# Performance work log

Hardware: AMD Instinct MI355X
Metric: run time of the kernel (lower is better)

The kernel has to match this reference:

```python
import jax, jax.numpy as jnp
import numpy as np


def setup_inputs() -> dict:
    key = jax.random.key(0)
    k1, k2, k3, k4 = jax.random.split(key, 4)
    n1, n2, d, num_types = 8192, 8192, 512, 64
    return {
        "input1": jax.random.normal(k1, (n1, d), dtype=jnp.float32),
        "input2": jax.random.normal(k2, (n2, d), dtype=jnp.float32),
        "weight": jax.random.normal(k3, (num_types, d), dtype=jnp.float32),
        "bias": jax.random.uniform(k4, (1,), dtype=jnp.float32),
        "type_index": 3,
    }


def reference(input1, input2, weight, bias, type_index):
    # DistMult score: (input1 * w_r) @ input2^T + bias.
    # Original builds diag(w_r) and does a dense d x d GEMM; the faithful
    # math is an elementwise row-scale followed by one GEMM.
    w_r = weight[type_index]                      # [d]
    scaled = input1 * w_r[None, :]                # [n1, d]
    out = scaled @ input2.T + bias                # [n1, n2]
    return out  # act is identity
```

## Files before the change

### kernel.cpp

```cpp
#include <hip/hip_runtime.h>


#define N1 8192
#define N2 8192
#define DK 512
#define BM 128
#define BN 128
#define BK 32

typedef short bf16x8 __attribute__((ext_vector_type(8)));
typedef float f32x4 __attribute__((ext_vector_type(4)));

__device__ __forceinline__ unsigned short f2bf(float f) {
    unsigned int u = __float_as_uint(f);
    u = (u + 0x7FFFu + ((u >> 16) & 1u)) >> 16;
    return (unsigned short)u;
}

__global__ __launch_bounds__(256) void convert_kernel(
        const float* __restrict__ in1, const float* __restrict__ in2,
        const float* __restrict__ weight, const int* __restrict__ type_index,
        unsigned short* __restrict__ a_bf, unsigned short* __restrict__ b_bf) {
    const int QA = N1 * DK / 4;
    int i = blockIdx.x * blockDim.x + threadIdx.x;
    if (i < QA) {
        float4 v = reinterpret_cast<const float4*>(in1)[i];
        int c4 = i & (DK / 4 - 1);
        float4 w = reinterpret_cast<const float4*>(weight + (size_t)(*type_index) * DK)[c4];
        ushort4 o;
        o.x = f2bf(v.x * w.x);
        o.y = f2bf(v.y * w.y);
        o.z = f2bf(v.z * w.z);
        o.w = f2bf(v.w * w.w);
        reinterpret_cast<ushort4*>(a_bf)[i] = o;
    } else {
        int j = i - QA;
        float4 v = reinterpret_cast<const float4*>(in2)[j];
        ushort4 o;
        o.x = f2bf(v.x);
        o.y = f2bf(v.y);
        o.z = f2bf(v.z);
        o.w = f2bf(v.w);
        reinterpret_cast<ushort4*>(b_bf)[j] = o;
    }
}

__global__ __launch_bounds__(256) void gemm_bt(
        const unsigned short* __restrict__ A, const unsigned short* __restrict__ B,
        const float* __restrict__ bias, float* __restrict__ C) {
    __shared__ __align__(16) unsigned short ldsA[BM * BK];
    __shared__ __align__(16) unsigned short ldsB[BN * BK];

    const int tid  = threadIdx.x;
    const int wave = tid >> 6;
    const int lane = tid & 63;
    const int quad = lane >> 4;
    const int r16  = lane & 15;
    const int wm   = wave & 1;
    const int wn   = wave >> 1;

    const int bm = blockIdx.y * BM;
    const int bn = blockIdx.x * BN;

    f32x4 acc[4][4];
#pragma unroll
    for (int i = 0; i < 4; ++i)
#pragma unroll
        for (int j = 0; j < 4; ++j)
            acc[i][j] = (f32x4){0.f, 0.f, 0.f, 0.f};

    const int srow = wave * 32 + (lane >> 2);
    const int scol = (lane & 3) * 8;
    const unsigned short* ag0 = A + (size_t)(bm + srow) * DK + scol;
    const unsigned short* ag1 = ag0 + 16 * DK;
    const unsigned short* bg0 = B + (size_t)(bn + srow) * DK + scol;
    const unsigned short* bg1 = bg0 + 16 * DK;

    unsigned short* la0 = &ldsA[wave * 1024];
    unsigned short* la1 = &ldsA[wave * 1024 + 512];
    unsigned short* lb0 = &ldsB[wave * 1024];
    unsigned short* lb1 = &ldsB[wave * 1024 + 512];

    for (int kt = 0; kt < DK; kt += BK) {
        __builtin_amdgcn_global_load_lds(ag0 + kt, la0, 16, 0, 0);
        __builtin_amdgcn_global_load_lds(ag1 + kt, la1, 16, 0, 0);
        __builtin_amdgcn_global_load_lds(bg0 + kt, lb0, 16, 0, 0);
        __builtin_amdgcn_global_load_lds(bg1 + kt, lb1, 16, 0, 0);
        __syncthreads();

        bf16x8 af[4], bfr[4];
#pragma unroll
        for (int mi = 0; mi < 4; ++mi)
            af[mi] = *(const bf16x8*)&ldsA[(wm * 64 + mi * 16 + r16) * BK + quad * 8];
#pragma unroll
        for (int ni = 0; ni < 4; ++ni)
            bfr[ni] = *(const bf16x8*)&ldsB[(wn * 64 + ni * 16 + r16) * BK + quad * 8];

#pragma unroll
        for (int mi = 0; mi < 4; ++mi)
#pragma unroll
            for (int ni = 0; ni < 4; ++ni)
                acc[mi][ni] = __builtin_amdgcn_mfma_f32_16x16x32_bf16(
                    af[mi], bfr[ni], acc[mi][ni], 0, 0, 0);
        __syncthreads();
    }

    const float bv = bias[0];
#pragma unroll
    for (int mi = 0; mi < 4; ++mi) {
        const int row0 = bm + wm * 64 + mi * 16 + quad * 4;
#pragma unroll
        for (int ni = 0; ni < 4; ++ni) {
            const int col = bn + wn * 64 + ni * 16 + r16;
#pragma unroll
            for (int r = 0; r < 4; ++r)
                C[(size_t)(row0 + r) * N2 + col] = acc[mi][ni][r] + bv;
        }
    }
}

__global__ void naive_kernel(const float* __restrict__ in1, const float* __restrict__ in2,
                             const float* __restrict__ weight, const int* __restrict__ type_index,
                             const float* __restrict__ bias, float* __restrict__ out) {
    int col = blockIdx.x * 16 + threadIdx.x;
    int row = blockIdx.y * 16 + threadIdx.y;
    const float* wr = weight + (size_t)(*type_index) * DK;
    float s = 0.f;
    for (int k = 0; k < DK; ++k)
        s += in1[(size_t)row * DK + k] * wr[k] * in2[(size_t)col * DK + k];
    out[(size_t)row * N2 + col] = s + bias[0];
}

extern "C" void kernel_launch(void* const* d_in, const int* in_sizes, int n_in,
                              void* d_out, int out_size, void* d_ws, size_t ws_size,
                              hipStream_t stream) {
    const float* in1  = (const float*)d_in[0];
    const float* in2  = (const float*)d_in[1];
    const float* wgt  = (const float*)d_in[2];
    const float* bias = (const float*)d_in[3];
    const int*   tix  = (const int*)d_in[4];
    float* out = (float*)d_out;

    const size_t need = 2ull * (N1 + N2) * DK;
    if (ws_size >= need) {
        unsigned short* a_bf = (unsigned short*)d_ws;
        unsigned short* b_bf = a_bf + (size_t)N1 * DK;

        const int total4 = (N1 + N2) * DK / 4;
        convert_kernel<<<total4 / 256, 256, 0, stream>>>(in1, in2, wgt, tix, a_bf, b_bf);

        dim3 grid(N2 / BN, N1 / BM);
        gemm_bt<<<grid, 256, 0, stream>>>(a_bf, b_bf, bias, out);
    } else {
        dim3 grid(N2 / 16, N1 / 16);
        dim3 blk(16, 16);
        naive_kernel<<<grid, blk, 0, stream>>>(in1, in2, wgt, tix, bias, out);
    }
}
```

Measured before the change: 348.9 us.

## Replace GEMM with 256x256 double-buffered swizzled-LDS kernel with interleaved loads

Adds a new bf16 MFMA GEMM that uses 256x256 output tiles, 512 threads and 128 KB of dynamic LDS. K-tiles of 64 are double-buffered and their async global-to-LDS loads are interleaved between MFMA quarter-blocks, with explicit waitcnt and setprio control. It also XOR-swizzles the LDS layout to reduce bank conflicts and remaps block IDs for L2 locality. The goal is more data reuse per tile and overlap of memory traffic with compute. In exchange, occupancy is lower, register pressure is high, and a hipFuncSetAttribute call is made on every launch.

After: 388.2 us. +11.2%, slower.

```diff
diff --git a/kernel.cpp b/kernel.cpp
--- a/kernel.cpp
+++ b/kernel.cpp
@@ -4,9 +4,12 @@
 #define N1 8192
 #define N2 8192
 #define DK 512
+
 #define BM 128
 #define BN 128
 #define BK 32
+
+#define NT (DK / 64)
 
 typedef short bf16x8 __attribute__((ext_vector_type(8)));
 typedef float f32x4 __attribute__((ext_vector_type(4)));
@@ -45,6 +48,139 @@
     }
 }
 
+#define FENCE() asm volatile("" ::: "memory")
+#define LGKM(n) asm volatile("s_waitcnt lgkmcnt(" #n ")" ::: "memory")
+#define VMC(n)  asm volatile("s_waitcnt vmcnt(" #n ")" ::: "memory")
+#define SB0()   __builtin_amdgcn_sched_barrier(0)
+#define BARR()  do { FENCE(); __builtin_amdgcn_s_barrier(); FENCE(); } while (0)
+
+#define MMAQ(M0, N0)                                                                  \
+    do {                                                                              \
+        __builtin_amdgcn_s_setprio(1);                                                \
+        _Pragma("unroll") for (int mi_ = 0; mi_ < 4; ++mi_)                           \
+        _Pragma("unroll") for (int ni_ = 0; ni_ < 2; ++ni_)                           \
+        _Pragma("unroll") for (int kk_ = 0; kk_ < 2; ++kk_)                           \
+            acc[(M0) + mi_][(N0) + ni_] = __builtin_amdgcn_mfma_f32_16x16x32_bf16(    \
+                af[(M0) + mi_][kk_], bfr[(N0) + ni_][kk_], acc[(M0) + mi_][(N0) + ni_], 0, 0, 0); \
+        __builtin_amdgcn_s_setprio(0);                                                \
+    } while (0)
+
+#define STAGE(srcp, matbase, h, T) do {                                               \
+    char* _d = sm + (matbase) + (((T) & 1) * 32768) + (h) * 16384 + wave * 1024;      \
+    __builtin_amdgcn_global_load_lds(                                                 \
+        (const unsigned int*)((srcp) + (size_t)(T) * 128), (unsigned int*)_d, 16, 0, 0); \
+    __builtin_amdgcn_global_load_lds(                                                 \
+        (const unsigned int*)((srcp) + (size_t)(T) * 128 + 65536),                    \
+        (unsigned int*)(_d + 8192), 16, 0, 0);                                        \
+} while (0)
+
+__global__ __launch_bounds__(512, 2) void gemm_256(
+        const unsigned short* __restrict__ A, const unsigned short* __restrict__ B,
+        const float* __restrict__ bias, float* __restrict__ C) {
+    extern __shared__ char sm[];
+    const int tid  = threadIdx.x;
+    const int wave = tid >> 6;
+    const int lane = tid & 63;
+    const int quad = lane >> 4;
+    const int r16  = lane & 15;
+    const int wm   = wave >> 2;
+    const int wn   = wave & 3;
+
+    const int bid = blockIdx.x;
+    const int swz = (bid & 7) * 128 + (bid >> 3);
+    const int bm = (swz >> 5) * 256;
+    const int bn = (swz & 31) * 256;
+
+    const int rowh = tid >> 3;
+    const int colb = ((tid & 7) * 16) ^ (((tid >> 5) & 1) << 5);
+    const char* sA0 = (const char*)A + ((size_t)(bm +       rowh) * DK) * 2 + colb;
+    const char* sA1 = (const char*)A + ((size_t)(bm + 128 + rowh) * DK) * 2 + colb;
+    const char* sB0 = (const char*)B + ((size_t)(bn +       rowh) * DK) * 2 + colb;
+    const char* sB1 = (const char*)B + ((size_t)(bn + 128 + rowh) * DK) * 2 + colb;
+
+    f32x4 acc[8][4];
+#pragma unroll
+    for (int i = 0; i < 8; ++i)
+#pragma unroll
+        for (int j = 0; j < 4; ++j)
+            acc[i][j] = (f32x4){0.f, 0.f, 0.f, 0.f};
+
+    const int flip32 = ((r16 >> 2) & 1) << 5;
+    const int xoff   = (r16 * 128 + quad * 16) ^ flip32;
+
+    STAGE(sA0, 0,     0, 0); STAGE(sA1, 0,     1, 0);
+    STAGE(sB0, 65536, 0, 0); STAGE(sB1, 65536, 1, 0);
+    STAGE(sA0, 0,     0, 1); STAGE(sA1, 0,     1, 1);
+    STAGE(sB0, 65536, 0, 1);
+    VMC(6);
+    BARR();
+
+#pragma unroll 1
+    for (int t = 0; t < NT; ++t) {
+        const char* bA = sm + ((t & 1) * 32768) + wm * 16384 + xoff;
+        const char* bB = sm + 65536 + ((t & 1) * 32768) + wn * 8192 + xoff;
+        bf16x8 af[8][2], bfr[4][2];
+
+#pragma unroll
+        for (int mi = 0; mi < 8; ++mi) {
+            af[mi][0] = *(const bf16x8*)(bA + mi * 2048);
+            af[mi][1] = *(const bf16x8*)(bA + mi * 2048 + 64);
+        }
+        FENCE();
+#pragma unroll
+        for (int ni = 0; ni < 2; ++ni) {
+            bfr[ni][0] = *(const bf16x8*)(bB + ni * 2048);
+            bfr[ni][1] = *(const bf16x8*)(bB + ni * 2048 + 64);
+        }
+        FENCE();
+#pragma unroll
+        for (int ni = 2; ni < 4; ++ni) {
+            bfr[ni][0] = *(const bf16x8*)(bB + ni * 2048);
+            bfr[ni][1] = *(const bf16x8*)(bB + ni * 2048 + 64);
+        }
+        FENCE();
+        if (t + 1 < NT) STAGE(sB1, 65536, 1, t + 1);
+        BARR();
+        LGKM(4); SB0();
+        MMAQ(0, 0);
+        BARR();
+
+        if (t + 2 < NT) STAGE(sA0, 0, 0, t + 2);
+        BARR();
+        MMAQ(4, 0);
+        BARR();
+
+        if (t + 2 < NT) STAGE(sA1, 0, 1, t + 2);
+        BARR();
+        LGKM(0); SB0();
+        MMAQ(0, 2);
+        BARR();
+
+        if (t + 2 < NT) STAGE(sB0, 65536, 0, t + 2);
+        BARR();
+        MMAQ(4, 2);
+        if (t < NT - 2) { VMC(6); }
+        else if (t == NT - 2) { VMC(0); }
+        BARR();
+    }
+
+    const float bv = bias[0];
+#pragma unroll
+    for (int mi = 0; mi < 8; ++mi) {
+        const int row0 = bm + wm * 128 + mi * 16 + quad * 4;
+#pragma unroll
+        for (int ni = 0; ni < 4; ++ni) {
+            const int col = bn + wn * 64 + ni * 16 + r16;
+#pragma unroll
+            for (int r = 0; r < 4; ++r)
+                C[(size_t)(row0 + r) * N2 + col] = acc[mi][ni][r] + bv;
+        }
+    }
+}
+
+#undef STAGE
+#undef MMAQ
+
 __global__ __launch_bounds__(256) void gemm_bt(
         const unsigned short* __restrict__ A, const unsigned short* __restrict__ B,
         const float* __restrict__ bias, float* __restrict__ C) {
@@ -149,8 +285,15 @@
         const int total4 = (N1 + N2) * DK / 4;
         convert_kernel<<<total4 / 256, 256, 0, stream>>>(in1, in2, wgt, tix, a_bf, b_bf);
 
-        dim3 grid(N2 / BN, N1 / BM);
-        gemm_bt<<<grid, 256, 0, stream>>>(a_bf, b_bf, bias, out);
+        hipError_t e = hipFuncSetAttribute(
+            reinterpret_cast<const void*>(gemm_256),
+            hipFuncAttributeMaxDynamicSharedMemorySize, 131072);
+        if (e == hipSuccess) {
+            gemm_256<<<dim3(1024), dim3(512), 131072, stream>>>(a_bf, b_bf, bias, out);
+        } else {
+            dim3 grid(N2 / BN, N1 / BM);
+            gemm_bt<<<grid, 256, 0, stream>>>(a_bf, b_bf, bias, out);
+        }
     } else {
         dim3 grid(N2 / 16, N1 / 16);
         dim3 blk(16, 16);
```

## Fuse bf16 conversion into a 256x256 register-prefetched MFMA GEMM

Applied to the files above, without the earlier changes.

Replaces the separate convert kernel and bf16 GEMM with one fused kernel. It loads fp32 inputs, scales A by the weight row, converts to bf16 in registers and writes to XOR-swizzled, double-buffered LDS while MFMAs run on the current buffer. The kernel also uses 256x256 tiles with 8 waves, a grid swizzle for L2 locality, and s_setprio around the MFMA blocks. This drops the workspace round trip and one launch. In exchange, fp32 inputs are re-read and re-converted by every tile that uses them, register pressure rises, and 128KB of dynamic LDS limits occupancy.

After: 807.0 us. 131% more time.

```diff
diff --git a/kernel.cpp b/kernel.cpp
--- a/kernel.cpp
+++ b/kernel.cpp
@@ -4,104 +4,336 @@
 #define N1 8192
 #define N2 8192
 #define DK 512
-#define BM 128
-#define BN 128
-#define BK 32
+#define NT 8
 
 typedef short bf16x8 __attribute__((ext_vector_type(8)));
-typedef float f32x4 __attribute__((ext_vector_type(4)));
-
-__device__ __forceinline__ unsigned short f2bf(float f) {
+typedef float f32x4  __attribute__((ext_vector_type(4)));
+
+__device__ __forceinline__ unsigned int f2bf_u(float f) {
     unsigned int u = __float_as_uint(f);
-    u = (u + 0x7FFFu + ((u >> 16) & 1u)) >> 16;
-    return (unsigned short)u;
-}
-
-__global__ __launch_bounds__(256) void convert_kernel(
+    return (u + 0x7FFFu + ((u >> 16) & 1u)) >> 16;
+}
+__device__ __forceinline__ unsigned int pk2(float lo, float hi) {
+    return f2bf_u(lo) | (f2bf_u(hi) << 16);
+}
+
+__global__ __launch_bounds__(512, 2) void fused_gemm_256(
         const float* __restrict__ in1, const float* __restrict__ in2,
         const float* __restrict__ weight, const int* __restrict__ type_index,
-        unsigned short* __restrict__ a_bf, unsigned short* __restrict__ b_bf) {
-    const int QA = N1 * DK / 4;
-    int i = blockIdx.x * blockDim.x + threadIdx.x;
-    if (i < QA) {
-        float4 v = reinterpret_cast<const float4*>(in1)[i];
-        int c4 = i & (DK / 4 - 1);
-        float4 w = reinterpret_cast<const float4*>(weight + (size_t)(*type_index) * DK)[c4];
-        ushort4 o;
-        o.x = f2bf(v.x * w.x);
-        o.y = f2bf(v.y * w.y);
-        o.z = f2bf(v.z * w.z);
-        o.w = f2bf(v.w * w.w);
-        reinterpret_cast<ushort4*>(a_bf)[i] = o;
-    } else {
-        int j = i - QA;
-        float4 v = reinterpret_cast<const float4*>(in2)[j];
-        ushort4 o;
-        o.x = f2bf(v.x);
-        o.y = f2bf(v.y);
-        o.z = f2bf(v.z);
-        o.w = f2bf(v.w);
-        reinterpret_cast<ushort4*>(b_bf)[j] = o;
-    }
-}
-
-__global__ __launch_bounds__(256) void gemm_bt(
-        const unsigned short* __restrict__ A, const unsigned short* __restrict__ B,
         const float* __restrict__ bias, float* __restrict__ C) {
-    __shared__ __align__(16) unsigned short ldsA[BM * BK];
-    __shared__ __align__(16) unsigned short ldsB[BN * BK];
-
+    extern __shared__ char sm[];
     const int tid  = threadIdx.x;
     const int wave = tid >> 6;
     const int lane = tid & 63;
     const int quad = lane >> 4;
     const int r16  = lane & 15;
-    const int wm   = wave & 1;
-    const int wn   = wave >> 1;
-
-    const int bm = blockIdx.y * BM;
-    const int bn = blockIdx.x * BN;
-
-    f32x4 acc[4][4];
-#pragma unroll
-    for (int i = 0; i < 4; ++i)
+    const int wm   = wave >> 2;
+    const int wn   = wave & 3;
+
+    const int bid = blockIdx.x;
+    const int swz = (bid & 7) * 128 + (bid >> 3);
+    const int bm = (swz >> 5) * 256;
+    const int bn = (swz & 31) * 256;
+
+    const float* wr = weight + (size_t)(*type_index) * DK;
+
+    const int rq = tid >> 3;
+    const int c8 = (tid & 7) * 8;
+    const float* gA = in1 + (size_t)(bm + rq) * DK + c8;
+    const float* gB = in2 + (size_t)(bn + rq) * DK + c8;
+    const int wflip = ((tid >> 5) & 3) << 5;
+    const int woff  = rq * 128 + (((tid & 7) * 16) ^ wflip);
+
+    const int rflip = ((r16 >> 2) & 3) << 5;
+    const int col0  = (quad * 16) ^ rflip;
+    const int col1  = (64 + quad * 16) ^ rflip;
+    const int rbaseA = (wm * 128 + r16) * 128;
+    const int rbaseB = (wn * 64  + r16) * 128;
+
+    f32x4 acc[8][4];
+#pragma unroll
+    for (int i = 0; i < 8; ++i)
 #pragma unroll
         for (int j = 0; j < 4; ++j)
             acc[i][j] = (f32x4){0.f, 0.f, 0.f, 0.f};
 
-    const int srow = wave * 32 + (lane >> 2);
-    const int scol = (lane & 3) * 8;
-    const unsigned short* ag0 = A + (size_t)(bm + srow) * DK + scol;
-    const unsigned short* ag1 = ag0 + 16 * DK;
-    const unsigned short* bg0 = B + (size_t)(bn + srow) * DK + scol;
-    const unsigned short* bg1 = bg0 + 16 * DK;
-
-    unsigned short* la0 = &ldsA[wave * 1024];
-    unsigned short* la1 = &ldsA[wave * 1024 + 512];
-    unsigned short* lb0 = &ldsB[wave * 1024];
-    unsigned short* lb1 = &ldsB[wave * 1024 + 512];
-
-    for (int kt = 0; kt < DK; kt += BK) {
-        __builtin_amdgcn_global_load_lds(ag0 + kt, la0, 16, 0, 0);
-        __builtin_amdgcn_global_load_lds(ag1 + kt, la1, 16, 0, 0);
-        __builtin_amdgcn_global_load_lds(bg0 + kt, lb0, 16, 0, 0);
-        __builtin_amdgcn_global_load_lds(bg1 + kt, lb1, 16, 0, 0);
-        __syncthreads();
-
-        bf16x8 af[4], bfr[4];
-#pragma unroll
-        for (int mi = 0; mi < 4; ++mi)
-            af[mi] = *(const bf16x8*)&ldsA[(wm * 64 + mi * 16 + r16) * BK + quad * 8];
+    {
+        float4 w0 = *(const float4*)(wr + c8);
+        float4 w1 = *(const float4*)(wr + c8 + 4);
+        float4 ra0[4], ra1[4], rb0[4], rb1[4];
+#pragma unroll
+        for (int p = 0; p < 4; ++p) {
+            const float* gap = gA + (size_t)(p * 64) * DK;
+            const float* gbp = gB + (size_t)(p * 64) * DK;
+            ra0[p] = *(const float4*)gap;  ra1[p] = *(const float4*)(gap + 4);
+            rb0[p] = *(const float4*)gbp;  rb1[p] = *(const float4*)(gbp + 4);
+        }
+#pragma unroll
+        for (int p = 0; p < 4; ++p) {
+            uint4 da, db;
+            da.x = pk2(ra0[p].x * w0.x, ra0[p].y * w0.y);
+            da.y = pk2(ra0[p].z * w0.z, ra0[p].w * w0.w);
+            da.z = pk2(ra1[p].x * w1.x, ra1[p].y * w1.y);
+            da.w = pk2(ra1[p].z * w1.z, ra1[p].w * w1.w);
+            *(uint4*)(sm + woff + p * 8192) = da;
+            db.x = pk2(rb0[p].x, rb0[p].y);
+            db.y = pk2(rb0[p].z, rb0[p].w);
+            db.z = pk2(rb1[p].x, rb1[p].y);
+            db.w = pk2(rb1[p].z, rb1[p].w);
+            *(uint4*)(sm + 65536 + woff + p * 8192) = db;
+        }
+    }
+    __syncthreads();
+
+#pragma unroll 1
+    for (int t = 0; t < NT; ++t) {
+        const char* bufA = sm + (t & 1) * 32768;
+        const char* bufB = sm + 65536 + (t & 1) * 32768;
+        char* nA = sm + ((t + 1) & 1) * 32768;
+        char* nB = sm + 65536 + ((t + 1) & 1) * 32768;
+        const bool pf = (t + 1 < NT);
+
+        float4 w0, w1, ra0[4], ra1[4], rb0[4], rb1[4];
+        if (pf) {
+            const float* wp  = wr + (t + 1) * 64 + c8;
+            w0 = *(const float4*)wp;
+            w1 = *(const float4*)(wp + 4);
+            const float* gap = gA + (t + 1) * 64;
+#pragma unroll
+            for (int p = 0; p < 4; ++p) {
+                ra0[p] = *(const float4*)(gap + (size_t)(p * 64) * DK);
+                ra1[p] = *(const float4*)(gap + (size_t)(p * 64) * DK + 4);
+            }
+            const float* gbp = gB + (t + 1) * 64;
+#pragma unroll
+            for (int p = 0; p < 4; ++p) {
+                rb0[p] = *(const float4*)(gbp + (size_t)(p * 64) * DK);
+                rb1[p] = *(const float4*)(gbp + (size_t)(p * 64) * DK + 4);
+            }
+        }
+
+        bf16x8 af0[8], bf0[4];
+#pragma unroll
+        for (int mi = 0; mi < 8; ++mi)
+            af0[mi] = *(const bf16x8*)(bufA + rbaseA + mi * 2048 + col0);
 #pragma unroll
         for (int ni = 0; ni < 4; ++ni)
-            bfr[ni] = *(const bf16x8*)&ldsB[(wn * 64 + ni * 16 + r16) * BK + quad * 8];
-
-#pragma unroll
-        for (int mi = 0; mi < 4; ++mi)
+            bf0[ni] = *(const bf16x8*)(bufB + rbaseB + ni * 2048 + col0);
+        __builtin_amdgcn_s_setprio(1);
+#pragma unroll
+        for (int mi = 0; mi < 8; ++mi)
 #pragma unroll
             for (int ni = 0; ni < 4; ++ni)
                 acc[mi][ni] = __builtin_amdgcn_mfma_f32_16x16x32_bf16(
-                    af[mi], bfr[ni], acc[mi][ni], 0, 0, 0);
+                    af0[mi], bf0[ni], acc[mi][ni], 0, 0, 0);
+        __builtin_amdgcn_s_setprio(0);
+
+        if (pf) {
+#pragma unroll
+            for (int p = 0; p < 4; ++p) {
+                uint4 da;
+                da.x = pk2(ra0[p].x * w0.x, ra0[p].y * w0.y);
+                da.y = pk2(ra0[p].z * w0.z, ra0[p].w * w0.w);
+                da.z = pk2(ra1[p].x * w1.x, ra1[p].y * w1.y);
+                da.w = pk2(ra1[p].z * w1.z, ra1[p].w * w1.w);
+                *(uint4*)(nA + woff + p * 8192) = da;
+            }
+        }
+
+        bf16x8 af1[8], bf1[4];
+#pragma unroll
+        for (int mi = 0; mi < 8; ++mi)
+            af1[mi] = *(const bf16x8*)(bufA + rbaseA + mi * 2048 + col1);
+#pragma unroll
+        for (int ni = 0; ni < 4; ++ni)
+            bf1[ni] = *(const bf16x8*)(bufB + rbaseB + ni * 2048 + col1);
+        __builtin_amdgcn_s_setprio(1);
+#pragma unroll
+        for (int mi = 0; mi < 8; ++mi)
+#pragma unroll
+            for (int ni = 0; ni < 4; ++ni)
+                acc[mi][ni] = __builtin_amdgcn_mfma_f32_16x16x32_bf16(
+                    af1[mi], bf1[ni], acc[mi][ni], 0, 0, 0);
+        __builtin_amdgcn_s_setprio(0);
+
+        if (pf) {
+#pragma unroll
+            for (int p = 0; p < 4; ++p) {
+                uint4 db;
+                db.x = pk2(rb0[p].x, rb0[p].y);
+                db.y = pk2(rb0[p].z, rb0[p].w);
+                db.z = pk2(rb1[p].x, rb1[p].y);
+                db.w = pk2(rb1[p].z, rb1[p].w);
+                *(uint4*)(nB + woff + p * 8192) = db;
+            }
+        }
+        __syncthreads();
+    }
+
+    const float bv = bias[0];
+#pragma unroll
+    for (int mi = 0; mi < 8; ++mi) {
+        const int row0 = bm + wm * 128 + mi * 16 + quad * 4;
+#pragma unroll
+        for (int ni = 0; ni < 4; ++ni) {
+            const int col = bn + wn * 64 + ni * 16 + r16;
+#pragma unroll
+            for (int r = 0; r < 4; ++r)
+                C[(size_t)(row0 + r) * N2 + col] = acc[mi][ni][r] + bv;
+        }
+    }
+}
+
+__global__ __launch_bounds__(512, 4) void fused_gemm_128(
+        const float* __restrict__ in1, const float* __restrict__ in2,
+        const float* __restrict__ weight, const int* __restrict__ type_index,
+        const float* __restrict__ bias, float* __restrict__ C) {
+    __shared__ __align__(16) char sm[65536];
+    const int tid  = threadIdx.x;
+    const int wave = tid >> 6;
+    const int lane = tid & 63;
+    const int quad = lane >> 4;
+    const int r16  = lane & 15;
+    const int wm   = wave >> 2;
+    const int wn   = wave & 3;
+
+    const int bid = blockIdx.x;
+    const int swz = (bid & 7) * 512 + (bid >> 3);
+    const int bm = (swz >> 6) * 128;
+    const int bn = (swz & 63) * 128;
+
+    const float* wr = weight + (size_t)(*type_index) * DK;
+
+    const int rq = tid >> 3;
+    const int c8 = (tid & 7) * 8;
+    const float* gA = in1 + (size_t)(bm + rq) * DK + c8;
+    const float* gB = in2 + (size_t)(bn + rq) * DK + c8;
+    const int wflip = ((tid >> 5) & 3) << 5;
+    const int woff  = rq * 128 + (((tid & 7) * 16) ^ wflip);
+
+    const int rflip = ((r16 >> 2) & 3) << 5;
+    const int col0  = (quad * 16) ^ rflip;
+    const int col1  = (64 + quad * 16) ^ rflip;
+    const int rbaseA = (wm * 64 + r16) * 128;
+    const int rbaseB = (wn * 32 + r16) * 128;
+
+    f32x4 acc[4][2];
+#pragma unroll
+    for (int i = 0; i < 4; ++i)
+#pragma unroll
+        for (int j = 0; j < 2; ++j)
+            acc[i][j] = (f32x4){0.f, 0.f, 0.f, 0.f};
+
+    {
+        float4 w0 = *(const float4*)(wr + c8);
+        float4 w1 = *(const float4*)(wr + c8 + 4);
+        float4 ra0[2], ra1[2], rb0[2], rb1[2];
+#pragma unroll
+        for (int p = 0; p < 2; ++p) {
+            const float* gap = gA + (size_t)(p * 64) * DK;
+            const float* gbp = gB + (size_t)(p * 64) * DK;
+            ra0[p] = *(const float4*)gap;  ra1[p] = *(const float4*)(gap + 4);
+            rb0[p] = *(const float4*)gbp;  rb1[p] = *(const float4*)(gbp + 4);
+        }
+#pragma unroll
+        for (int p = 0; p < 2; ++p) {
+            uint4 da, db;
+            da.x = pk2(ra0[p].x * w0.x, ra0[p].y * w0.y);
+            da.y = pk2(ra0[p].z * w0.z, ra0[p].w * w0.w);
+            da.z = pk2(ra1[p].x * w1.x, ra1[p].y * w1.y);
+            da.w = pk2(ra1[p].z * w1.z, ra1[p].w * w1.w);
+            *(uint4*)(sm + woff + p * 8192) = da;
+            db.x = pk2(rb0[p].x, rb0[p].y);
+            db.y = pk2(rb0[p].z, rb0[p].w);
+            db.z = pk2(rb1[p].x, rb1[p].y);
+            db.w = pk2(rb1[p].z, rb1[p].w);
+            *(uint4*)(sm + 32768 + woff + p * 8192) = db;
+        }
+    }
+    __syncthreads();
+
+#pragma unroll 1
+    for (int t = 0; t < NT; ++t) {
+        const char* bufA = sm + (t & 1) * 16384;
+        const char* bufB = sm + 32768 + (t & 1) * 16384;
+        char* nA = sm + ((t + 1) & 1) * 16384;
+        char* nB = sm + 32768 + ((t + 1) & 1) * 16384;
+        const bool pf = (t + 1 < NT);
+
+        float4 w0, w1, ra0[2], ra1[2], rb0[2], rb1[2];
+        if (pf) {
+            const float* wp  = wr + (t + 1) * 64 + c8;
+            w0 = *(const float4*)wp;
+            w1 = *(const float4*)(wp + 4);
+            const float* gap = gA + (t + 1) * 64;
+            const float* gbp = gB + (t + 1) * 64;
+#pragma unroll
+            for (int p = 0; p < 2; ++p) {
+                ra0[p] = *(const float4*)(gap + (size_t)(p * 64) * DK);
+                ra1[p] = *(const float4*)(gap + (size_t)(p * 64) * DK + 4);
+            }
+#pragma unroll
+            for (int p = 0; p < 2; ++p) {
+                rb0[p] = *(const float4*)(gbp + (size_t)(p * 64) * DK);
+                rb1[p] = *(const float4*)(gbp + (size_t)(p * 64) * DK + 4);
+            }
+        }
+
+        bf16x8 af0[4], bf0[2];
+#pragma unroll
+        for (int mi = 0; mi < 4; ++mi)
+            af0[mi] = *(const bf16x8*)(bufA + rbaseA + mi * 2048 + col0);
+#pragma unroll
+        for (int ni = 0; ni < 2; ++ni)
+            bf0[ni] = *(const bf16x8*)(bufB + rbaseB + ni * 2048 + col0);
+        __builtin_amdgcn_s_setprio(1);
+#pragma unroll
+        for (int mi = 0; mi < 4; ++mi)
+#pragma unroll
+            for (int ni = 0; ni < 2; ++ni)
+                acc[mi][ni] = __builtin_amdgcn_mfma_f32_16x16x32_bf16(
+                    af0[mi], bf0[ni], acc[mi][ni], 0, 0, 0);
+        __builtin_amdgcn_s_setprio(0);
+
+        if (pf) {
+#pragma unroll
+            for (int p = 0; p < 2; ++p) {
+                uint4 da;
+                da.x = pk2(ra0[p].x * w0.x, ra0[p].y * w0.y);
+                da.y = pk2(ra0[p].z * w0.z, ra0[p].w * w0.w);
+                da.z = pk2(ra1[p].x * w1.x, ra1[p].y * w1.y);
+                da.w = pk2(ra1[p].z * w1.z, ra1[p].w * w1.w);
+                *(uint4*)(nA + woff + p * 8192) = da;
+            }
+        }
+
+        bf16x8 af1[4], bf1[2];
+#pragma unroll
+        for (int mi = 0; mi < 4; ++mi)
+            af1[mi] = *(const bf16x8*)(bufA + rbaseA + mi * 2048 + col1);
+#pragma unroll
+        for (int ni = 0; ni < 2; ++ni)
+            bf1[ni] = *(const bf16x8*)(bufB + rbaseB + ni * 2048 + col1);
+        __builtin_amdgcn_s_setprio(1);
+#pragma unroll
+        for (int mi = 0; mi < 4; ++mi)
+#pragma unroll
+            for (int ni = 0; ni < 2; ++ni)
+                acc[mi][ni] = __builtin_amdgcn_mfma_f32_16x16x32_bf16(
+                    af1[mi], bf1[ni], acc[mi][ni], 0, 0, 0);
+        __builtin_amdgcn_s_setprio(0);
+
+        if (pf) {
+#pragma unroll
+            for (int p = 0; p < 2; ++p) {
+                uint4 db;
+                db.x = pk2(rb0[p].x, rb0[p].y);
+                db.y = pk2(rb0[p].z, rb0[p].w);
+                db.z = pk2(rb1[p].x, rb1[p].y);
+                db.w = pk2(rb1[p].z, rb1[p].w);
+                *(uint4*)(nB + woff + p * 8192) = db;
+            }
+        }
         __syncthreads();
     }
 
@@ -110,25 +342,13 @@
     for (int mi = 0; mi < 4; ++mi) {
         const int row0 = bm + wm * 64 + mi * 16 + quad * 4;
 #pragma unroll
-        for (int ni = 0; ni < 4; ++ni) {
-            const int col = bn + wn * 64 + ni * 16 + r16;
+        for (int ni = 0; ni < 2; ++ni) {
+            const int col = bn + wn * 32 + ni * 16 + r16;
 #pragma unroll
             for (int r = 0; r < 4; ++r)
                 C[(size_t)(row0 + r) * N2 + col] = acc[mi][ni][r] + bv;
         }
     }
-}
-
-__global__ void naive_kernel(const float* __restrict__ in1, const float* __restrict__ in2,
-                             const float* __restrict__ weight, const int* __restrict__ type_index,
-                             const float* __restrict__ bias, float* __restrict__ out) {
-    int col = blockIdx.x * 16 + threadIdx.x;
-    int row = blockIdx.y * 16 + threadIdx.y;
-    const float* wr = weight + (size_t)(*type_index) * DK;
-    float s = 0.f;
-    for (int k = 0; k < DK; ++k)
-        s += in1[(size_t)row * DK + k] * wr[k] * in2[(size_t)col * DK + k];
-    out[(size_t)row * N2 + col] = s + bias[0];
 }
 
 extern "C" void kernel_launch(void* const* d_in, const int* in_sizes, int n_in,
@@ -141,19 +361,16 @@
     const int*   tix  = (const int*)d_in[4];
     float* out = (float*)d_out;
 
-    const size_t need = 2ull * (N1 + N2) * DK;
-    if (ws_size >= need) {
-        unsigned short* a_bf = (unsigned short*)d_ws;
-        unsigned short* b_bf = a_bf + (size_t)N1 * DK;
-
-        const int total4 = (N1 + N2) * DK / 4;
-        convert_kernel<<<total4 / 256, 256, 0, stream>>>(in1, in2, wgt, tix, a_bf, b_bf);
-
-        dim3 grid(N2 / BN, N1 / BM);
-        gemm_bt<<<grid, 256, 0, stream>>>(a_bf, b_bf, bias, out);
+    (void)d_ws; (void)ws_size;
+
+    hipError_t e = hipFuncSetAttribute(
+        reinterpret_cast<const void*>(fused_gemm_256),
+        hipFuncAttributeMaxDynamicSharedMemorySize, 131072);
+    if (e == hipSuccess) {
+        fused_gemm_256<<<dim3(1024), dim3(512), 131072, stream>>>(
+            in1, in2, wgt, tix, bias, out);
     } else {
-        dim3 grid(N2 / 16, N1 / 16);
-        dim3 blk(16, 16);
-        naive_kernel<<<grid, blk, 0, stream>>>(in1, in2, wgt, tix, bias, out);
-    }
-}
+        fused_gemm_128<<<dim3(4096), dim3(512), 0, stream>>>(
+            in1, in2, wgt, tix, bias, out);
+    }
+}
```

## Double GEMM K-tile to 64 and XOR-swizzle LDS layout to avoid bank conflicts

Applied to the files above, without the earlier changes.

Raises the K tile from 32 to 64 so each barrier pair covers twice the MFMA work, halving the number of sync rounds in the main loop. Each wave now loads 8 rows of 64 bf16 per global_load_lds instruction, four times, with the 16-byte column chunk XOR-permuted by row. The fragment reads apply the same XOR so ds_read_b128 accesses spread across LDS banks. LDS use doubles to 32 KB per block, which may lower occupancy, and the loop still has no double buffering.

New measurement: 340.1 us. 1.03x faster.

```diff
diff --git a/kernel.cpp b/kernel.cpp
--- a/kernel.cpp
+++ b/kernel.cpp
@@ -6,7 +6,7 @@
 #define DK 512
 #define BM 128
 #define BN 128
-#define BK 32
+#define BK 64
 
 typedef short bf16x8 __attribute__((ext_vector_type(8)));
 typedef float f32x4 __attribute__((ext_vector_type(4)));
@@ -69,39 +69,57 @@
         for (int j = 0; j < 4; ++j)
             acc[i][j] = (f32x4){0.f, 0.f, 0.f, 0.f};
 
-    const int srow = wave * 32 + (lane >> 2);
-    const int scol = (lane & 3) * 8;
-    const unsigned short* ag0 = A + (size_t)(bm + srow) * DK + scol;
-    const unsigned short* ag1 = ag0 + 16 * DK;
-    const unsigned short* bg0 = B + (size_t)(bn + srow) * DK + scol;
-    const unsigned short* bg1 = bg0 + 16 * DK;
+    const int l8   = lane >> 3;
+    const int perm = (lane & 7) ^ l8;
+    const int srow = wave * 32 + l8;
+    const int scol = perm * 8;
+    const unsigned short* ag = A + (size_t)(bm + srow) * DK + scol;
+    const unsigned short* bg = B + (size_t)(bn + srow) * DK + scol;
+    unsigned short* la = &ldsA[wave * 2048];
+    unsigned short* lb = &ldsB[wave * 2048];
 
-    unsigned short* la0 = &ldsA[wave * 1024];
-    unsigned short* la1 = &ldsA[wave * 1024 + 512];
-    unsigned short* lb0 = &ldsB[wave * 1024];
-    unsigned short* lb1 = &ldsB[wave * 1024 + 512];
+    const int rs   = r16 & 7;
+    const int col0 = ((0 * 4 + quad) ^ rs) * 8;
+    const int col1 = ((1 * 4 + quad) ^ rs) * 8;
 
     for (int kt = 0; kt < DK; kt += BK) {
-        __builtin_amdgcn_global_load_lds(ag0 + kt, la0, 16, 0, 0);
-        __builtin_amdgcn_global_load_lds(ag1 + kt, la1, 16, 0, 0);
-        __builtin_amdgcn_global_load_lds(bg0 + kt, lb0, 16, 0, 0);
-        __builtin_amdgcn_global_load_lds(bg1 + kt, lb1, 16, 0, 0);
+#pragma unroll
+        for (int i = 0; i < 4; ++i) {
+            __builtin_amdgcn_global_load_lds(ag + kt + i * 8 * DK, la + i * 512, 16, 0, 0);
+            __builtin_amdgcn_global_load_lds(bg + kt + i * 8 * DK, lb + i * 512, 16, 0, 0);
+        }
         __syncthreads();
 
-        bf16x8 af[4], bfr[4];
+        {
+            bf16x8 af[4], bfr[4];
 #pragma unroll
-        for (int mi = 0; mi < 4; ++mi)
-            af[mi] = *(const bf16x8*)&ldsA[(wm * 64 + mi * 16 + r16) * BK + quad * 8];
-#pragma unroll
-        for (int ni = 0; ni < 4; ++ni)
-            bfr[ni] = *(const bf16x8*)&ldsB[(wn * 64 + ni * 16 + r16) * BK + quad * 8];
-
-#pragma unroll
-        for (int mi = 0; mi < 4; ++mi)
+            for (int mi = 0; mi < 4; ++mi)
+                af[mi] = *(const bf16x8*)&ldsA[(wm * 64 + mi * 16 + r16) * BK + col0];
 #pragma unroll
             for (int ni = 0; ni < 4; ++ni)
-                acc[mi][ni] = __builtin_amdgcn_mfma_f32_16x16x32_bf16(
-                    af[mi], bfr[ni], acc[mi][ni], 0, 0, 0);
+                bfr[ni] = *(const bf16x8*)&ldsB[(wn * 64 + ni * 16 + r16) * BK + col0];
+#pragma unroll
+            for (int mi = 0; mi < 4; ++mi)
+#pragma unroll
+                for (int ni = 0; ni < 4; ++ni)
+                    acc[mi][ni] = __builtin_amdgcn_mfma_f32_16x16x32_bf16(
+                        af[mi], bfr[ni], acc[mi][ni], 0, 0, 0);
+        }
+        {
+            bf16x8 af[4], bfr[4];
+#pragma unroll
+            for (int mi = 0; mi < 4; ++mi)
+                af[mi] = *(const bf16x8*)&ldsA[(wm * 64 + mi * 16 + r16) * BK + col1];
+#pragma unroll
+            for (int ni = 0; ni < 4; ++ni)
+                bfr[ni] = *(const bf16x8*)&ldsB[(wn * 64 + ni * 16 + r16) * BK + col1];
+#pragma unroll
+            for (int mi = 0; mi < 4; ++mi)
+#pragma unroll
+                for (int ni = 0; ni < 4; ++ni)
+                    acc[mi][ni] = __builtin_amdgcn_mfma_f32_16x16x32_bf16(
+                        af[mi], bfr[ni], acc[mi][ni], 0, 0, 0);
+        }
         __syncthreads();
     }
 
```
